# Kernel tuning notes

Hardware: AMD Instinct MI355X
Metric: run time of the kernel (lower is better)

The kernel has to match this reference:

```python
import jax, jax.numpy as jnp
import numpy as np
import math

B, S, DM, H = 4, 2048, 1024, 16
HD = DM // H

def setup_inputs() -> dict:
    key = jax.random.key(0)
    ks = jax.random.split(key, 12)
    def lin(k, din, dout):
        bound = 1.0 / math.sqrt(din)
        kw, kb = jax.random.split(k)
        W = jax.random.uniform(kw, (din, dout), jnp.float32, -bound, bound)
        b = jax.random.uniform(kb, (dout,), jnp.float32, -bound, bound)
        return W, b
    Wq, bq = lin(ks[0], DM, DM)
    Wk, bk = lin(ks[1], DM, DM)
    Wv, bv = lin(ks[2], DM, DM)
    Wo, bo = lin(ks[3], DM, DM)
    return {
        "Q": jax.random.normal(ks[4], (B, S, DM), jnp.float32),
        "K": jax.random.normal(ks[5], (B, S, DM), jnp.float32),
        "V": jax.random.normal(ks[6], (B, S, DM), jnp.float32),
        "mask": jnp.ones((B, S), jnp.int32),
        "Wq": Wq, "bq": bq, "Wk": Wk, "bk": bk,
        "Wv": Wv, "bv": bv, "Wo": Wo, "bo": bo,
    }

def reference(Q, K, V, mask, Wq, bq, Wk, bk, Wv, bv, Wo, bo):
    N, qlen, dm = Q.shape
    klen = K.shape[1]
    q = (Q @ Wq + bq).reshape(N, qlen, H, HD)
    k = (K @ Wk + bk).reshape(N, klen, H, HD)
    v = (V @ Wv + bv).reshape(N, klen, H, HD)
    # scores: [B, q, H, k]
    dot = jnp.einsum('bqhd,bkhd->bqhk', q, k) / math.sqrt(HD)
    # mask is 2-D (N, klen): broadcast as (N, 1, 1, klen); positions where mask==0 are masked
    m = (mask == 0)[:, None, None, :]
    dot = jnp.where(m, -jnp.inf, dot)
    weights = jax.nn.softmax(dot.astype(jnp.float32), axis=-1).astype(dot.dtype)
    out = jnp.einsum('bqhk,bkhd->bqhd', weights, v).reshape(N, qlen, dm)
    return out @ Wo + bo
```

## Files before the change

### kernel.cpp

```cpp
#include <hip/hip_runtime.h>
#include <math.h>

#define B_  4
#define S_  2048
#define DM_ 1024
#define H_  16
#define HD_ 64

typedef float f32x4 __attribute__((ext_vector_type(4)));
typedef short bf16x8 __attribute__((ext_vector_type(8)));

#define MFMA16(a, b, c) __builtin_amdgcn_mfma_f32_16x16x32_bf16((a), (b), (c), 0, 0, 0)

static __device__ __forceinline__ unsigned short f2bf(float f) {
    union { float f; unsigned int i; } c; c.f = f;
    unsigned int u = c.i;
    return (unsigned short)((u + 0x7fffu + ((u >> 16) & 1u)) >> 16);
}
static __device__ __forceinline__ unsigned int f2u(float f) {
    union { float f; unsigned int u; } c; c.f = f; return c.u;
}

static __device__ __forceinline__ void async16(const void* g, void* l) {
    __builtin_amdgcn_global_load_lds(
        (__attribute__((address_space(1))) void*)(void*)g,
        (__attribute__((address_space(3))) void*)l, 16, 0, 0);
}

__global__ __launch_bounds__(256) void cast3_bf16(
    const float* __restrict__ q, const float* __restrict__ k,
    const float* __restrict__ v,
    unsigned short* __restrict__ qo, unsigned short* __restrict__ ko,
    unsigned short* __restrict__ vo) {
    const int z = blockIdx.z;
    const float* in = z == 0 ? q : (z == 1 ? k : v);
    unsigned short* out = z == 0 ? qo : (z == 1 ? ko : vo);
    int idx = (blockIdx.x * 256 + threadIdx.x) * 8;
    float4 a = *(const float4*)(in + idx);
    float4 b = *(const float4*)(in + idx + 4);
    *(ushort4*)(out + idx)     = make_ushort4(f2bf(a.x), f2bf(a.y), f2bf(a.z), f2bf(a.w));
    *(ushort4*)(out + idx + 4) = make_ushort4(f2bf(b.x), f2bf(b.y), f2bf(b.z), f2bf(b.w));
}

__global__ __launch_bounds__(256) void maskprep(
    const int* __restrict__ mask, float* __restrict__ maddf,
    unsigned int* __restrict__ flags) {
    int i = blockIdx.x * 256 + threadIdx.x;
    int m = mask[i];
    maddf[i] = m ? 0.f : -__builtin_inff();
    unsigned long long bal = __ballot(m != 0);
    if ((threadIdx.x & 63) == 0)
        flags[i >> 6] = (bal == 0xFFFFFFFFFFFFFFFFull) ? 1u : 0u;
}

__global__ __launch_bounds__(256) void wcast4_t(
    const float* __restrict__ w0, const float* __restrict__ w1,
    const float* __restrict__ w2, const float* __restrict__ w3,
    unsigned short* __restrict__ o0, unsigned short* __restrict__ o1,
    unsigned short* __restrict__ o2, unsigned short* __restrict__ o3) {
    __shared__ float tile[64][65];
    const int z = blockIdx.z;
    const float* W = z == 0 ? w0 : (z == 1 ? w1 : (z == 2 ? w2 : w3));
    unsigned short* Wt = z == 0 ? o0 : (z == 1 ? o1 : (z == 2 ? o2 : o3));
    const int t = threadIdx.x;
    const int k0 = blockIdx.y * 64, n0 = blockIdx.x * 64;
    const int r = t >> 4, c4 = (t & 15) * 4;
    #pragma unroll
    for (int s = 0; s < 4; ++s) {
        float4 f = *(const float4*)(W + (size_t)(k0 + s * 16 + r) * DM_ + n0 + c4);
        tile[s * 16 + r][c4 + 0] = f.x; tile[s * 16 + r][c4 + 1] = f.y;
        tile[s * 16 + r][c4 + 2] = f.z; tile[s * 16 + r][c4 + 3] = f.w;
    }
    __syncthreads();
    #pragma unroll
    for (int s = 0; s < 4; ++s) {
        int n = s * 16 + r;
        ushort4 o = make_ushort4(f2bf(tile[c4 + 0][n]), f2bf(tile[c4 + 1][n]),
                                 f2bf(tile[c4 + 2][n]), f2bf(tile[c4 + 3][n]));
        *(ushort4*)(Wt + (size_t)(n0 + n) * DM_ + k0 + c4) = o;
    }
}

static __device__ __forceinline__ void gemm_body(
    const unsigned short* __restrict__ A,
    const unsigned short* __restrict__ Wt,
    const float* __restrict__ bias,
    void* __restrict__ outp, int mode, float oscale,
    unsigned short* As, unsigned short* Bs)
{
    const int t = threadIdx.x;
    const int w = t >> 6, l = t & 63;
    const int quad = l >> 4, l16 = l & 15;
    const int wr = w >> 1, wc = w & 1;
    const int m0 = blockIdx.y * 128, n0 = blockIdx.x * 128;

    const int srow8 = l >> 3;
    const int sch   = (l & 7) ^ srow8;
    const unsigned short* ag = A  + (size_t)(m0 + w * 32 + srow8) * DM_ + sch * 8;
    const unsigned short* bg = Wt + (size_t)(n0 + w * 32 + srow8) * DM_ + sch * 8;

    const f32x4 fz = {0.f, 0.f, 0.f, 0.f};
    f32x4 acc[4][4];
    #pragma unroll
    for (int i = 0; i < 4; ++i)
        #pragma unroll
        for (int j = 0; j < 4; ++j) acc[i][j] = fz;

    const int rsw = l16 & 7;
    for (int k0 = 0; k0 < DM_; k0 += 64) {
        __syncthreads();
        #pragma unroll
        for (int s = 0; s < 4; ++s) {
            async16(ag + k0 + (size_t)(s * 8) * DM_, &As[(w * 32 + s * 8) * 64]);
            async16(bg + k0 + (size_t)(s * 8) * DM_, &Bs[(w * 32 + s * 8) * 64]);
        }
        __syncthreads();
        #pragma unroll
        for (int c = 0; c < 2; ++c) {
            const int csw = ((c * 4 + quad) ^ rsw) * 8;
            bf16x8 af[4], bfr[4];
            #pragma unroll
            for (int i = 0; i < 4; ++i)
                af[i] = *(const bf16x8*)&As[(wr * 64 + i * 16 + l16) * 64 + csw];
            #pragma unroll
            for (int j = 0; j < 4; ++j)
                bfr[j] = *(const bf16x8*)&Bs[(wc * 64 + j * 16 + l16) * 64 + csw];
            #pragma unroll
            for (int i = 0; i < 4; ++i)
                #pragma unroll
                for (int j = 0; j < 4; ++j)
                    acc[i][j] = MFMA16(af[i], bfr[j], acc[i][j]);
        }
    }

    float bv[4];
    #pragma unroll
    for (int j = 0; j < 4; ++j) bv[j] = bias[n0 + wc * 64 + j * 16 + l16];

    if (mode == 2) {
        float* out = (float*)outp;
        #pragma unroll
        for (int i = 0; i < 4; ++i)
            #pragma unroll
            for (int j = 0; j < 4; ++j) {
                int col = n0 + wc * 64 + j * 16 + l16;
                #pragma unroll
                for (int r = 0; r < 4; ++r) {
                    int row = m0 + wr * 64 + i * 16 + quad * 4 + r;
                    out[(size_t)row * DM_ + col] = acc[i][j][r] + bv[j];
                }
            }
    } else if (mode == 0) {
        unsigned short* out = (unsigned short*)outp;
        #pragma unroll
        for (int i = 0; i < 4; ++i)
            #pragma unroll
            for (int j = 0; j < 4; ++j) {
                int col = n0 + wc * 64 + j * 16 + l16;
                int h = col >> 6, d = col & 63;
                #pragma unroll
                for (int r = 0; r < 4; ++r) {
                    int row = m0 + wr * 64 + i * 16 + quad * 4 + r;
                    int bb = row >> 11, ss = row & (S_ - 1);
                    out[(((size_t)bb * H_ + h) * S_ + ss) * HD_ + d] =
                        f2bf((acc[i][j][r] + bv[j]) * oscale);
                }
            }
    } else {
        unsigned short* out = (unsigned short*)outp;
        #pragma unroll
        for (int i = 0; i < 4; ++i)
            #pragma unroll
            for (int j = 0; j < 4; ++j) {
                int col = n0 + wc * 64 + j * 16 + l16;
                int h = col >> 6, d = col & 63;
                int row0 = m0 + wr * 64 + i * 16 + quad * 4;
                int bb = row0 >> 11, ss = row0 & (S_ - 1);
                ushort4 o = make_ushort4(f2bf(acc[i][j][0] + bv[j]),
                                         f2bf(acc[i][j][1] + bv[j]),
                                         f2bf(acc[i][j][2] + bv[j]),
                                         f2bf(acc[i][j][3] + bv[j]));
                *(ushort4*)(out + (((size_t)bb * H_ + h) * HD_ + d) * S_ + ss) = o;
            }
    }
}

__global__ __launch_bounds__(256) void gemm_qkv3(
    const unsigned short* __restrict__ Qc, const unsigned short* __restrict__ Kc,
    const unsigned short* __restrict__ Vc,
    const unsigned short* __restrict__ Wqt, const unsigned short* __restrict__ Wkt,
    const unsigned short* __restrict__ Wvt,
    const float* __restrict__ bq, const float* __restrict__ bk,
    const float* __restrict__ bvp,
    unsigned short* __restrict__ qh, unsigned short* __restrict__ kh,
    unsigned short* __restrict__ vth)
{
    __shared__ unsigned short As[128 * 64];
    __shared__ unsigned short Bs[128 * 64];
    const int z = blockIdx.z;
    const unsigned short* A  = z == 0 ? Qc  : (z == 1 ? Kc  : Vc);
    const unsigned short* Wt = z == 0 ? Wqt : (z == 1 ? Wkt : Wvt);
    const float* bias        = z == 0 ? bq  : (z == 1 ? bk  : bvp);
    void* out                = z == 0 ? (void*)qh : (z == 1 ? (void*)kh : (void*)vth);
    const float qsc = 0.18033688011112042f;
    gemm_body(A, Wt, bias, out, z == 2 ? 1 : 0, z == 0 ? qsc : 1.0f, As, Bs);
}

__global__ __launch_bounds__(256) void gemm_omfma(
    const unsigned short* __restrict__ A, const unsigned short* __restrict__ Wt,
    const float* __restrict__ bias, float* __restrict__ out)
{
    __shared__ unsigned short As[128 * 64];
    __shared__ unsigned short Bs[128 * 64];
    gemm_body(A, Wt, bias, out, 2, 1.0f, As, Bs);
}

template<bool MASKED>
static __device__ __forceinline__ void softmax_store(
    const f32x4* sc, const float (*madd)[4], unsigned short* Pg,
    int l16, int quad, int rsw)
{
    #pragma unroll
    for (int kk = 0; kk < 4; ++kk) {
        int kb = (kk * 2 + (quad >> 1)) ^ rsw;
        #pragma unroll
        for (int rp = 0; rp < 2; ++rp) {
            float a0 = sc[kk][rp * 2 + 0], a1 = sc[kk][rp * 2 + 1];
            if (MASKED) { a0 += madd[kk][rp * 2 + 0]; a1 += madd[kk][rp * 2 + 1]; }
            float p0 = __builtin_amdgcn_exp2f(a0);
            float p1 = __builtin_amdgcn_exp2f(a1);
            unsigned int pk = __builtin_amdgcn_perm(f2u(p1), f2u(p0), 0x07060302u);
            *(unsigned int*)&Pg[l16 * 64 + kb * 8 + (quad & 1) * 4 + rp * 2] = pk;
        }
    }
}

__global__ __launch_bounds__(256) void attn_mfma(
    const unsigned short* __restrict__ q,
    const unsigned short* __restrict__ k,
    const unsigned short* __restrict__ vt,
    const float* __restrict__ maddf,
    const unsigned int* __restrict__ flags,
    unsigned short* __restrict__ out)
{
    __shared__ unsigned short Ks[2][64 * 64];
    __shared__ unsigned short Vs[2][64 * 64];
    __shared__ unsigned short Ps[4][2][16 * 64];
    const int t = threadIdx.x;
    const int w = t >> 6, l = t & 63;
    const int quad = l >> 4, l16 = l & 15;

    const int bid = blockIdx.x;
    const int swz = (bid & 7) * 128 + (bid >> 3);
    const int qb = swz & 15, h = (swz >> 4) & 15, b = swz >> 8;
    const int q0 = qb * 128;
    const size_t hb = ((size_t)b * H_ + h) * S_;

    const int srow8 = l >> 3;
    const int sch   = (l & 7) ^ srow8;
    const int rsw   = l16 & 7;

    const unsigned short* qg = q + (hb + q0) * HD_;
    bf16x8 qf[2][2];
    #pragma unroll
    for (int g = 0; g < 2; ++g)
        #pragma unroll
        for (int c = 0; c < 2; ++c)
            qf[g][c] = *(const bf16x8*)(qg +
                (size_t)(w * 32 + g * 16 + l16) * HD_ + (c * 4 + quad) * 8);

    const bf16x8 onesf = {(short)0x3F80, (short)0x3F80, (short)0x3F80, (short)0x3F80,
                          (short)0x3F80, (short)0x3F80, (short)0x3F80, (short)0x3F80};

    const f32x4 fz = {0.f, 0.f, 0.f, 0.f};
    f32x4 o[2][4];
    f32x4 ol[2] = {fz, fz};
    #pragma unroll
    for (int g = 0; g < 2; ++g)
        #pragma unroll
        for (int jv = 0; jv < 4; ++jv) o[g][jv] = fz;

    const unsigned short* kg0 = k + hb * HD_;
    const unsigned short* vg0 = vt + ((size_t)b * H_ + h) * HD_ * S_;

    auto stage = [&](int d, int kt) {
        #pragma unroll
        for (int s = 0; s < 2; ++s) {
            int r0 = w * 16 + s * 8;
            int rr = r0 + srow8;
            async16(kg0 + (size_t)(kt * 64 + rr) * HD_ + sch * 8, &Ks[d][r0 * 64]);
            async16(vg0 + (size_t)rr * S_ + kt * 64 + sch * 8, &Vs[d][r0 * 64]);
        }
    };

    stage(0, 0);
    int cur = 0;
    for (int kt = 0; kt < S_ / 64; ++kt) {
        __syncthreads();
        if (kt + 1 < S_ / 64) stage(cur ^ 1, kt + 1);

        const int allv = flags[b * (S_ / 64) + kt];
        float madd[4][4];
        if (!allv) {
            #pragma unroll
            for (int kk = 0; kk < 4; ++kk) {
                float4 mv = *(const float4*)&maddf[(size_t)b * S_ + kt * 64 + kk * 16 + quad * 4];
                madd[kk][0] = mv.x; madd[kk][1] = mv.y;
                madd[kk][2] = mv.z; madd[kk][3] = mv.w;
            }
        }

        const unsigned short* Kc = &Ks[cur][0];
        bf16x8 kf[4][2];
        #pragma unroll
        for (int kk = 0; kk < 4; ++kk) {
            int row = kk * 16 + l16;
            #pragma unroll
            for (int c = 0; c < 2; ++c)
                kf[kk][c] = *(const bf16x8*)&Kc[row * 64 + (((c * 4 + quad) ^ rsw) * 8)];
        }
        #pragma unroll
        for (int g = 0; g < 2; ++g) {
            f32x4 sc[4];
            #pragma unroll
            for (int kk = 0; kk < 4; ++kk) sc[kk] = fz;
            __builtin_amdgcn_s_setprio(1);
            #pragma unroll
            for (int kk = 0; kk < 4; ++kk) {
                sc[kk] = MFMA16(kf[kk][0], qf[g][0], sc[kk]);
                sc[kk] = MFMA16(kf[kk][1], qf[g][1], sc[kk]);
            }
            __builtin_amdgcn_s_setprio(0);
            if (allv) softmax_store<false>(sc, madd, &Ps[w][g][0], l16, quad, rsw);
            else      softmax_store<true >(sc, madd, &Ps[w][g][0], l16, quad, rsw);
        }

        const unsigned short* Vc = &Vs[cur][0];
        bf16x8 vfr[4][2];
        #pragma unroll
        for (int jv = 0; jv < 4; ++jv) {
            int row = jv * 16 + l16;
            #pragma unroll
            for (int c = 0; c < 2; ++c)
                vfr[jv][c] = *(const bf16x8*)&Vc[row * 64 + (((c * 4 + quad) ^ rsw) * 8)];
        }
        #pragma unroll
        for (int g = 0; g < 2; ++g) {
            bf16x8 pa0 = *(const bf16x8*)&Ps[w][g][l16 * 64 + ((quad ^ rsw) * 8)];
            bf16x8 pa1 = *(const bf16x8*)&Ps[w][g][l16 * 64 + (((4 + quad) ^ rsw) * 8)];
            __builtin_amdgcn_s_setprio(1);
            #pragma unroll
            for (int jv = 0; jv < 4; ++jv) {
                o[g][jv] = MFMA16(pa0, vfr[jv][0], o[g][jv]);
                o[g][jv] = MFMA16(pa1, vfr[jv][1], o[g][jv]);
            }
            ol[g] = MFMA16(pa0, onesf, ol[g]);
            ol[g] = MFMA16(pa1, onesf, ol[g]);
            __builtin_amdgcn_s_setprio(0);
        }
        cur ^= 1;
    }

    #pragma unroll
    for (int g = 0; g < 2; ++g) {
        float inv[4];
        #pragma unroll
        for (int r = 0; r < 4; ++r) inv[r] = 1.0f / ol[g][r];
        #pragma unroll
        for (int jv = 0; jv < 4; ++jv) {
            int col = h * HD_ + jv * 16 + l16;
            #pragma unroll
            for (int r = 0; r < 4; ++r) {
                int row = q0 + w * 32 + g * 16 + quad * 4 + r;
                out[((size_t)b * S_ + row) * DM_ + col] = f2bf(o[g][jv][r] * inv[r]);
            }
        }
    }
}

extern "C" void kernel_launch(void* const* d_in, const int* in_sizes, int n_in,
                              void* d_out, int out_size, void* d_ws, size_t ws_size,
                              hipStream_t stream) {
    const float* Q    = (const float*)d_in[0];
    const float* K    = (const float*)d_in[1];
    const float* V    = (const float*)d_in[2];
    const int*   mask = (const int*)d_in[3];
    const float* Wq   = (const float*)d_in[4];
    const float* bq   = (const float*)d_in[5];
    const float* Wk   = (const float*)d_in[6];
    const float* bk   = (const float*)d_in[7];
    const float* Wv   = (const float*)d_in[8];
    const float* bv   = (const float*)d_in[9];
    const float* Wo   = (const float*)d_in[10];
    const float* bo   = (const float*)d_in[11];

    char* ws = (char*)d_ws;
    const size_t MB = 1024 * 1024;
    unsigned short* Qc  = (unsigned short*)(ws);
    unsigned short* Kc  = (unsigned short*)(ws + 16 * MB);
    unsigned short* Vc  = (unsigned short*)(ws + 32 * MB);
    unsigned short* Wqt = (unsigned short*)(ws + 48 * MB);
    unsigned short* Wkt = (unsigned short*)(ws + 50 * MB);
    unsigned short* Wvt = (unsigned short*)(ws + 52 * MB);
    unsigned short* Wot = (unsigned short*)(ws + 54 * MB);
    unsigned short* qh  = (unsigned short*)(ws + 56 * MB);
    unsigned short* kh  = (unsigned short*)(ws + 72 * MB);
    unsigned short* vth = (unsigned short*)(ws + 88 * MB);
    unsigned short* ao  = (unsigned short*)(ws + 104 * MB);
    float*          maddf = (float*)(ws + 120 * MB);
    unsigned int*   flagsb = (unsigned int*)(ws + 120 * MB + 64 * 1024);

    cast3_bf16<<<dim3(4096, 1, 3), 256, 0, stream>>>(Q, K, V, Qc, Kc, Vc);
    maskprep<<<dim3((B_ * S_) / 256), 256, 0, stream>>>(mask, maddf, flagsb);
    wcast4_t<<<dim3(16, 16, 4), 256, 0, stream>>>(Wq, Wk, Wv, Wo, Wqt, Wkt, Wvt, Wot);
    gemm_qkv3<<<dim3(DM_ / 128, (B_ * S_) / 128, 3), 256, 0, stream>>>(
        Qc, Kc, Vc, Wqt, Wkt, Wvt, bq, bk, bv, qh, kh, vth);
    attn_mfma<<<dim3((S_ / 128) * H_ * B_), 256, 0, stream>>>(
        qh, kh, vth, maddf, flagsb, ao);
    gemm_omfma<<<dim3(DM_ / 128, (B_ * S_) / 128), 256, 0, stream>>>(ao, Wot, bo, (float*)d_out);
}
```

Before: 357.3 us.

## Double-buffer GEMM LDS staging, remap blocks per XCD, merge prep kernels

Merges the three prep kernels (activation cast, weight cast/transpose, mask prep) into one launch with block-index role dispatch. Double-buffers the GEMM LDS tiles so the async global-to-LDS loads for the next k-step are issued before computing the current one, which removes one barrier per iteration. Also remaps 1-D block ids so consecutive tiles sharing A rows land on the same XCD for better L2 reuse. This doubles LDS use per GEMM block to 64KB, which may lower occupancy.

Measured after the change: 342.6 us. 4.1% less time.

```diff
diff --git a/kernel.cpp b/kernel.cpp
--- a/kernel.cpp
+++ b/kernel.cpp
@@ -27,57 +27,56 @@
         (__attribute__((address_space(3))) void*)l, 16, 0, 0);
 }
 
-__global__ __launch_bounds__(256) void cast3_bf16(
-    const float* __restrict__ q, const float* __restrict__ k,
-    const float* __restrict__ v,
-    unsigned short* __restrict__ qo, unsigned short* __restrict__ ko,
-    unsigned short* __restrict__ vo) {
-    const int z = blockIdx.z;
-    const float* in = z == 0 ? q : (z == 1 ? k : v);
-    unsigned short* out = z == 0 ? qo : (z == 1 ? ko : vo);
-    int idx = (blockIdx.x * 256 + threadIdx.x) * 8;
-    float4 a = *(const float4*)(in + idx);
-    float4 b = *(const float4*)(in + idx + 4);
-    *(ushort4*)(out + idx)     = make_ushort4(f2bf(a.x), f2bf(a.y), f2bf(a.z), f2bf(a.w));
-    *(ushort4*)(out + idx + 4) = make_ushort4(f2bf(b.x), f2bf(b.y), f2bf(b.z), f2bf(b.w));
-}
-
-__global__ __launch_bounds__(256) void maskprep(
-    const int* __restrict__ mask, float* __restrict__ maddf,
-    unsigned int* __restrict__ flags) {
-    int i = blockIdx.x * 256 + threadIdx.x;
-    int m = mask[i];
-    maddf[i] = m ? 0.f : -__builtin_inff();
-    unsigned long long bal = __ballot(m != 0);
-    if ((threadIdx.x & 63) == 0)
-        flags[i >> 6] = (bal == 0xFFFFFFFFFFFFFFFFull) ? 1u : 0u;
-}
-
-__global__ __launch_bounds__(256) void wcast4_t(
+__global__ __launch_bounds__(256) void prep_all(
+    const float* __restrict__ Q, const float* __restrict__ K,
+    const float* __restrict__ V, const int* __restrict__ mask,
     const float* __restrict__ w0, const float* __restrict__ w1,
     const float* __restrict__ w2, const float* __restrict__ w3,
+    unsigned short* __restrict__ qo, unsigned short* __restrict__ ko,
+    unsigned short* __restrict__ vo,
     unsigned short* __restrict__ o0, unsigned short* __restrict__ o1,
-    unsigned short* __restrict__ o2, unsigned short* __restrict__ o3) {
+    unsigned short* __restrict__ o2, unsigned short* __restrict__ o3,
+    float* __restrict__ maddf, unsigned int* __restrict__ flags)
+{
     __shared__ float tile[64][65];
-    const int z = blockIdx.z;
-    const float* W = z == 0 ? w0 : (z == 1 ? w1 : (z == 2 ? w2 : w3));
-    unsigned short* Wt = z == 0 ? o0 : (z == 1 ? o1 : (z == 2 ? o2 : o3));
-    const int t = threadIdx.x;
-    const int k0 = blockIdx.y * 64, n0 = blockIdx.x * 64;
-    const int r = t >> 4, c4 = (t & 15) * 4;
-    #pragma unroll
-    for (int s = 0; s < 4; ++s) {
-        float4 f = *(const float4*)(W + (size_t)(k0 + s * 16 + r) * DM_ + n0 + c4);
-        tile[s * 16 + r][c4 + 0] = f.x; tile[s * 16 + r][c4 + 1] = f.y;
-        tile[s * 16 + r][c4 + 2] = f.z; tile[s * 16 + r][c4 + 3] = f.w;
-    }
-    __syncthreads();
-    #pragma unroll
-    for (int s = 0; s < 4; ++s) {
-        int n = s * 16 + r;
-        ushort4 o = make_ushort4(f2bf(tile[c4 + 0][n]), f2bf(tile[c4 + 1][n]),
-                                 f2bf(tile[c4 + 2][n]), f2bf(tile[c4 + 3][n]));
-        *(ushort4*)(Wt + (size_t)(n0 + n) * DM_ + k0 + c4) = o;
+    const int id = blockIdx.x, t = threadIdx.x;
+    if (id < 12288) {
+        const int z = id >> 12, x = id & 4095;
+        const float* in = z == 0 ? Q : (z == 1 ? K : V);
+        unsigned short* out = z == 0 ? qo : (z == 1 ? ko : vo);
+        int idx = (x * 256 + t) * 8;
+        float4 a = *(const float4*)(in + idx);
+        float4 b = *(const float4*)(in + idx + 4);
+        *(ushort4*)(out + idx)     = make_ushort4(f2bf(a.x), f2bf(a.y), f2bf(a.z), f2bf(a.w));
+        *(ushort4*)(out + idx + 4) = make_ushort4(f2bf(b.x), f2bf(b.y), f2bf(b.z), f2bf(b.w));
+    } else if (id < 13312) {
+        const int rr = id - 12288;
+        const int z = rr >> 8, ky = (rr >> 4) & 15, nx = rr & 15;
+        const float* W = z == 0 ? w0 : (z == 1 ? w1 : (z == 2 ? w2 : w3));
+        unsigned short* Wt = z == 0 ? o0 : (z == 1 ? o1 : (z == 2 ? o2 : o3));
+        const int k0 = ky * 64, n0 = nx * 64;
+        const int r = t >> 4, c4 = (t & 15) * 4;
+        #pragma unroll
+        for (int s = 0; s < 4; ++s) {
+            float4 f = *(const float4*)(W + (size_t)(k0 + s * 16 + r) * DM_ + n0 + c4);
+            tile[s * 16 + r][c4 + 0] = f.x; tile[s * 16 + r][c4 + 1] = f.y;
+            tile[s * 16 + r][c4 + 2] = f.z; tile[s * 16 + r][c4 + 3] = f.w;
+        }
+        __syncthreads();
+        #pragma unroll
+        for (int s = 0; s < 4; ++s) {
+            int n = s * 16 + r;
+            ushort4 o = make_ushort4(f2bf(tile[c4 + 0][n]), f2bf(tile[c4 + 1][n]),
+                                     f2bf(tile[c4 + 2][n]), f2bf(tile[c4 + 3][n]));
+            *(ushort4*)(Wt + (size_t)(n0 + n) * DM_ + k0 + c4) = o;
+        }
+    } else {
+        int i = (id - 13312) * 256 + t;
+        int m = mask[i];
+        maddf[i] = m ? 0.f : -__builtin_inff();
+        unsigned long long bal = __ballot(m != 0);
+        if ((t & 63) == 0)
+            flags[i >> 6] = (bal == 0xFFFFFFFFFFFFFFFFull) ? 1u : 0u;
     }
 }
 
@@ -85,14 +84,13 @@
     const unsigned short* __restrict__ A,
     const unsigned short* __restrict__ Wt,
     const float* __restrict__ bias,
-    void* __restrict__ outp, int mode, float oscale,
-    unsigned short* As, unsigned short* Bs)
+    void* __restrict__ outp, int mode, float oscale, int m0, int n0,
+    unsigned short (*As)[128 * 64], unsigned short (*Bs)[128 * 64])
 {
     const int t = threadIdx.x;
     const int w = t >> 6, l = t & 63;
     const int quad = l >> 4, l16 = l & 15;
     const int wr = w >> 1, wc = w & 1;
-    const int m0 = blockIdx.y * 128, n0 = blockIdx.x * 128;
 
     const int srow8 = l >> 3;
     const int sch   = (l & 7) ^ srow8;
@@ -107,30 +105,37 @@
         for (int j = 0; j < 4; ++j) acc[i][j] = fz;
 
     const int rsw = l16 & 7;
+
+    auto stageAB = [&](int d, int k0) {
+        #pragma unroll
+        for (int s = 0; s < 4; ++s) {
+            async16(ag + k0 + (size_t)(s * 8) * DM_, &As[d][(w * 32 + s * 8) * 64]);
+            async16(bg + k0 + (size_t)(s * 8) * DM_, &Bs[d][(w * 32 + s * 8) * 64]);
+        }
+    };
+
+    stageAB(0, 0);
+    int cur = 0;
     for (int k0 = 0; k0 < DM_; k0 += 64) {
         __syncthreads();
-        #pragma unroll
-        for (int s = 0; s < 4; ++s) {
-            async16(ag + k0 + (size_t)(s * 8) * DM_, &As[(w * 32 + s * 8) * 64]);
-            async16(bg + k0 + (size_t)(s * 8) * DM_, &Bs[(w * 32 + s * 8) * 64]);
-        }
-        __syncthreads();
+        if (k0 + 64 < DM_) stageAB(cur ^ 1, k0 + 64);
         #pragma unroll
         for (int c = 0; c < 2; ++c) {
             const int csw = ((c * 4 + quad) ^ rsw) * 8;
             bf16x8 af[4], bfr[4];
             #pragma unroll
             for (int i = 0; i < 4; ++i)
-                af[i] = *(const bf16x8*)&As[(wr * 64 + i * 16 + l16) * 64 + csw];
+                af[i] = *(const bf16x8*)&As[cur][(wr * 64 + i * 16 + l16) * 64 + csw];
             #pragma unroll
             for (int j = 0; j < 4; ++j)
-                bfr[j] = *(const bf16x8*)&Bs[(wc * 64 + j * 16 + l16) * 64 + csw];
+                bfr[j] = *(const bf16x8*)&Bs[cur][(wc * 64 + j * 16 + l16) * 64 + csw];
             #pragma unroll
             for (int i = 0; i < 4; ++i)
                 #pragma unroll
                 for (int j = 0; j < 4; ++j)
                     acc[i][j] = MFMA16(af[i], bfr[j], acc[i][j]);
         }
+        cur ^= 1;
     }
 
     float bv[4];
@@ -195,24 +200,30 @@
     unsigned short* __restrict__ qh, unsigned short* __restrict__ kh,
     unsigned short* __restrict__ vth)
 {
-    __shared__ unsigned short As[128 * 64];
-    __shared__ unsigned short Bs[128 * 64];
-    const int z = blockIdx.z;
+    __shared__ unsigned short As[2][128 * 64];
+    __shared__ unsigned short Bs[2][128 * 64];
+    const int id = blockIdx.x;
+    const int role = (id & 7) * 192 + (id >> 3);
+    const int z = role >> 9, r2 = role & 511;
+    const int m0 = (r2 >> 3) * 128, n0 = (r2 & 7) * 128;
     const unsigned short* A  = z == 0 ? Qc  : (z == 1 ? Kc  : Vc);
     const unsigned short* Wt = z == 0 ? Wqt : (z == 1 ? Wkt : Wvt);
     const float* bias        = z == 0 ? bq  : (z == 1 ? bk  : bvp);
     void* out                = z == 0 ? (void*)qh : (z == 1 ? (void*)kh : (void*)vth);
     const float qsc = 0.18033688011112042f;
-    gemm_body(A, Wt, bias, out, z == 2 ? 1 : 0, z == 0 ? qsc : 1.0f, As, Bs);
+    gemm_body(A, Wt, bias, out, z == 2 ? 1 : 0, z == 0 ? qsc : 1.0f, m0, n0, As, Bs);
 }
 
 __global__ __launch_bounds__(256) void gemm_omfma(
     const unsigned short* __restrict__ A, const unsigned short* __restrict__ Wt,
     const float* __restrict__ bias, float* __restrict__ out)
 {
-    __shared__ unsigned short As[128 * 64];
-    __shared__ unsigned short Bs[128 * 64];
-    gemm_body(A, Wt, bias, out, 2, 1.0f, As, Bs);
+    __shared__ unsigned short As[2][128 * 64];
+    __shared__ unsigned short Bs[2][128 * 64];
+    const int id = blockIdx.x;
+    const int role = (id & 7) * 64 + (id >> 3);
+    const int m0 = (role >> 3) * 128, n0 = (role & 7) * 128;
+    gemm_body(A, Wt, bias, out, 2, 1.0f, m0, n0, As, Bs);
 }
 
 template<bool MASKED>
@@ -410,12 +421,12 @@
     float*          maddf = (float*)(ws + 120 * MB);
     unsigned int*   flagsb = (unsigned int*)(ws + 120 * MB + 64 * 1024);
 
-    cast3_bf16<<<dim3(4096, 1, 3), 256, 0, stream>>>(Q, K, V, Qc, Kc, Vc);
-    maskprep<<<dim3((B_ * S_) / 256), 256, 0, stream>>>(mask, maddf, flagsb);
-    wcast4_t<<<dim3(16, 16, 4), 256, 0, stream>>>(Wq, Wk, Wv, Wo, Wqt, Wkt, Wvt, Wot);
-    gemm_qkv3<<<dim3(DM_ / 128, (B_ * S_) / 128, 3), 256, 0, stream>>>(
+    prep_all<<<dim3(13344), 256, 0, stream>>>(
+        Q, K, V, mask, Wq, Wk, Wv, Wo,
+        Qc, Kc, Vc, Wqt, Wkt, Wvt, Wot, maddf, flagsb);
+    gemm_qkv3<<<dim3(1536), 256, 0, stream>>>(
         Qc, Kc, Vc, Wqt, Wkt, Wvt, bq, bk, bv, qh, kh, vth);
-    attn_mfma<<<dim3((S_ / 128) * H_ * B_), 256, 0, stream>>>(
+    attn_mfma<<<dim3(1024), 256, 0, stream>>>(
         qh, kh, vth, maddf, flagsb, ao);
-    gemm_omfma<<<dim3(DM_ / 128, (B_ * S_) / 128), 256, 0, stream>>>(ao, Wot, bo, (float*)d_out);
-}
+    gemm_omfma<<<dim3(512), 256, 0, stream>>>(ao, Wot, bo, (float*)d_out);
+}
```
